# Performance work log

Measured on AMD Instinct MI355X. Metric: run time of the kernel, lower is better.

The kernel has to match this reference:

```python
import jax, jax.numpy as jnp
import numpy as np

B, H, S, D = 2, 16, 2048, 64
N_SINK = 1


def setup_inputs() -> dict:
    key = jax.random.key(0)
    kq, kk, ks = jax.random.split(key, 3)
    q = jax.random.normal(kq, (B, H, S, D), dtype=jnp.float32)
    k = jax.random.normal(kk, (B, H, S, D), dtype=jnp.float32)
    sinks = jax.random.normal(ks, (B, H, S, N_SINK), dtype=jnp.float32)
    return {"q": q, "k": k, "sinks": sinks}


def reference(q, k, sinks):
    # scores: [B,H,S,S] = q @ k^T
    scores = jnp.einsum("bhqd,bhkd->bhqk", q, k)
    # per-key norm ||k||, broadcast over query dim: [B,H,1,S]
    denom = jnp.sqrt(jnp.sum(k * k, axis=-1))[..., None, :]
    w = scores / denom
    # causal: zero (NOT -inf) above the diagonal, faithful to torch.tril
    w = jnp.tril(w)
    # append learned sink logits: [B,H,S,S+N_SINK]
    w = jnp.concatenate([w, sinks], axis=-1)
    return jax.nn.softmax(w, axis=-1)
```

## Files before the change

### kernel.cpp

```cpp
#include <hip/hip_runtime.h>
#include <hip/hip_fp16.h>
#include <math.h>

#define S 2048
#define D 64
#define BH 32
#define TILE 64
#define NT (S / TILE)
#define SP1 (S + 1)

typedef _Float16 f16;
typedef f16 f16x8 __attribute__((ext_vector_type(8)));
typedef f16 f16x4 __attribute__((ext_vector_type(4)));
typedef float f32x4 __attribute__((ext_vector_type(4)));

struct __attribute__((packed, aligned(4))) f4u { float x, y, z, w; };

#define LDS_PITCH 72

__global__ __launch_bounds__(256) void knorm_kernel(const float* __restrict__ k,
                                                    float* __restrict__ rinv) {
    int row  = (blockIdx.x * 256 + threadIdx.x) >> 6;
    int lane = threadIdx.x & 63;
    float v = k[(size_t)row * D + lane];
    float s = v * v;
    #pragma unroll
    for (int off = 32; off; off >>= 1) s += __shfl_xor(s, off);
    if (lane == 0) rinv[row] = 1.0f / sqrtf(s);
}

__global__ __launch_bounds__(256) void fused_kernel(
    const float* __restrict__ q, const float* __restrict__ k,
    const float* __restrict__ sinks, const float* __restrict__ rinv,
    float* __restrict__ out)
{
    __shared__ __align__(16) f16 qs[TILE * LDS_PITCH];
    __shared__ __align__(16) f16 ks[2][TILE * LDS_PITCH];
    __shared__ float ils[TILE];

    const int it = NT - 1 - blockIdx.x;
    const int bh = blockIdx.y;
    const int i0 = it * TILE;
    const int tid  = threadIdx.x;
    const int lane = tid & 63;
    const int w    = tid >> 6;
    const int m    = lane & 15;
    const int quad = lane >> 4;
    const int sr   = tid >> 4;
    const int sc4  = (tid & 15) * 4;

    const float* qbase = q + (size_t)bh * S * D;
    const float* kbase = k + (size_t)bh * S * D;
    const float* rbase = rinv + (size_t)bh * S;
    float* obase = out + (size_t)bh * S * SP1;

    float4 pre[4];

    auto loadk = [&](int jt) {
        const float* tb = kbase + (size_t)(jt * TILE) * D;
        #pragma unroll
        for (int rb = 0; rb < 4; rb++)
            pre[rb] = *(const float4*)(tb + (size_t)(rb * 16 + sr) * D + sc4);
    };
    auto writek = [&](int buf) {
        #pragma unroll
        for (int rb = 0; rb < 4; rb++) {
            float4 v = pre[rb];
            f16x4 hv; hv[0] = (f16)v.x; hv[1] = (f16)v.y; hv[2] = (f16)v.z; hv[3] = (f16)v.w;
            *(f16x4*)&ks[buf][(rb * 16 + sr) * LDS_PITCH + sc4] = hv;
        }
    };

    loadk(0);
    {
        #pragma unroll
        for (int rb = 0; rb < 4; rb++) {
            int row = rb * 16 + sr;
            float4 v = *(const float4*)(qbase + (size_t)(i0 + row) * D + sc4);
            f16x4 hv; hv[0] = (f16)v.x; hv[1] = (f16)v.y; hv[2] = (f16)v.z; hv[3] = (f16)v.w;
            *(f16x4*)&qs[row * LDS_PITCH + sc4] = hv;
        }
    }
    writek(0);
    __syncthreads();

    f16x8 a0 = *(const f16x8*)&qs[(w * 16 + m) * LDS_PITCH + 0  + quad * 8];
    f16x8 a1 = *(const f16x8*)&qs[(w * 16 + m) * LDS_PITCH + 32 + quad * 8];

    const int ib = i0 + w * 16 + quad * 4;

    float rowsum[4] = {0.f, 0.f, 0.f, 0.f};
    for (int jt = 0; jt <= it; jt++) {
        if (jt < it) loadk(jt + 1);
        const int buf = jt & 1;
        const bool diag = (jt == it);
        const int j0 = jt * TILE;
        #pragma unroll
        for (int st = 0; st < 4; st++) {
            f16x8 b0 = *(const f16x8*)&ks[buf][(st * 16 + m) * LDS_PITCH + 0  + quad * 8];
            f16x8 b1 = *(const f16x8*)&ks[buf][(st * 16 + m) * LDS_PITCH + 32 + quad * 8];
            f32x4 acc = {0.f, 0.f, 0.f, 0.f};
            acc = __builtin_amdgcn_mfma_f32_16x16x32_f16(a0, b0, acc, 0, 0, 0);
            acc = __builtin_amdgcn_mfma_f32_16x16x32_f16(a1, b1, acc, 0, 0, 0);
            const int j = j0 + st * 16 + m;
            const float rj = rbase[j];
            #pragma unroll
            for (int r = 0; r < 4; r++) {
                float e = __expf(acc[r] * rj);
                if (diag && j > ib + r) e = 0.0f;
                rowsum[r] += e;
            }
        }
        if (jt < it) writek((jt + 1) & 1);
        __syncthreads();
    }

    #pragma unroll
    for (int off = 1; off < 16; off <<= 1)
        #pragma unroll
        for (int r = 0; r < 4; r++) rowsum[r] += __shfl_xor(rowsum[r], off);

    if (m == 0) {
        #pragma unroll
        for (int r = 0; r < 4; r++) {
            int i = ib + r;
            float l = rowsum[r] + (float)(S - 1 - i) + __expf(sinks[bh * S + i]);
            ils[w * 16 + quad * 4 + r] = 1.0f / l;
        }
    }
    __syncthreads();

    if (tid < TILE) {
        int i = i0 + tid;
        obase[(size_t)i * SP1 + S] = __expf(sinks[bh * S + i]) * ils[tid];
    }

    float il[4];
    #pragma unroll
    for (int r = 0; r < 4; r++) il[r] = ils[w * 16 + quad * 4 + r];

    for (int jt = it; jt >= 0; jt--) {
        if (jt > 0) loadk(jt - 1);
        const int buf = jt & 1;
        const bool diag = (jt == it);
        const int j0 = jt * TILE;
        #pragma unroll
        for (int st = 0; st < 4; st++) {
            f16x8 b0 = *(const f16x8*)&ks[buf][(st * 16 + m) * LDS_PITCH + 0  + quad * 8];
            f16x8 b1 = *(const f16x8*)&ks[buf][(st * 16 + m) * LDS_PITCH + 32 + quad * 8];
            f32x4 acc = {0.f, 0.f, 0.f, 0.f};
            acc = __builtin_amdgcn_mfma_f32_16x16x32_f16(a0, b0, acc, 0, 0, 0);
            acc = __builtin_amdgcn_mfma_f32_16x16x32_f16(a1, b1, acc, 0, 0, 0);
            const int j = j0 + st * 16 + m;
            const float rj = rbase[j];
            #pragma unroll
            for (int r = 0; r < 4; r++) {
                float val = __expf(acc[r] * rj) * il[r];
                if (diag && j > ib + r) val = il[r];
                obase[(size_t)(ib + r) * SP1 + j] = val;
            }
        }
        if (jt > 0) writek((jt - 1) & 1);
        __syncthreads();
    }

    for (int jt = it + 1; jt < NT; jt++) {
        const int j0 = jt * TILE;
        #pragma unroll
        for (int rb = 0; rb < 4; rb++) {
            int row = w * 16 + rb * 4 + (lane >> 4);
            float v = ils[row];
            f4u vv = {v, v, v, v};
            *(f4u*)&obase[(size_t)(i0 + row) * SP1 + j0 + (lane & 15) * 4] = vv;
        }
    }
}

extern "C" void kernel_launch(void* const* d_in, const int* in_sizes, int n_in,
                              void* d_out, int out_size, void* d_ws, size_t ws_size,
                              hipStream_t stream) {
    const float* q     = (const float*)d_in[0];
    const float* k     = (const float*)d_in[1];
    const float* sinks = (const float*)d_in[2];
    float* out = (float*)d_out;

    float* rinv = (float*)d_ws;

    knorm_kernel<<<dim3(BH * S / 4), 256, 0, stream>>>(k, rinv);
    fused_kernel<<<dim3(NT, BH), 256, 0, stream>>>(q, k, sinks, rinv, out);
}
```

Measured before the change: 697.6 us.

## Pre-scale K to fp16 with folded norm, transpose MFMA for vectorized output stores

K is normalized, multiplied by log2(e) and converted to fp16 in a prep kernel, and Q is converted to fp16 in a separate prep kernel. The fused kernel then loads half-precision tiles directly, with no per-element rinv lookup, and uses exp2. The MFMA operands are swapped so each lane owns one query row and four consecutive keys, which allows a single 16-byte store per lane in the output pass instead of four scattered scalar stores. This adds an extra launch and a workspace round trip, and rounds the normalization and scale factor into fp16 K, which can slightly change accuracy.

```diff
diff --git a/kernel.cpp b/kernel.cpp
--- a/kernel.cpp
+++ b/kernel.cpp
@@ -8,6 +8,7 @@
 #define TILE 64
 #define NT (S / TILE)
 #define SP1 (S + 1)
+#define LOG2E 1.44269504088896f
 
 typedef _Float16 f16;
 typedef f16 f16x8 __attribute__((ext_vector_type(8)));
@@ -18,21 +19,31 @@
 
 #define LDS_PITCH 72
 
-__global__ __launch_bounds__(256) void knorm_kernel(const float* __restrict__ k,
-                                                    float* __restrict__ rinv) {
+__global__ __launch_bounds__(256) void prep_k(const float* __restrict__ k,
+                                              f16* __restrict__ kh) {
     int row  = (blockIdx.x * 256 + threadIdx.x) >> 6;
     int lane = threadIdx.x & 63;
     float v = k[(size_t)row * D + lane];
     float s = v * v;
     #pragma unroll
     for (int off = 32; off; off >>= 1) s += __shfl_xor(s, off);
-    if (lane == 0) rinv[row] = 1.0f / sqrtf(s);
+    kh[(size_t)row * D + lane] = (f16)(v * (1.0f / sqrtf(s)) * LOG2E);
+}
+
+__global__ __launch_bounds__(256) void prep_q(const float* __restrict__ q,
+                                              f16* __restrict__ qh) {
+    size_t t = (size_t)blockIdx.x * 256 + threadIdx.x;
+    const float4* src = (const float4*)(q + t * 8);
+    float4 v0 = src[0], v1 = src[1];
+    f16x8 h;
+    h[0] = (f16)v0.x; h[1] = (f16)v0.y; h[2] = (f16)v0.z; h[3] = (f16)v0.w;
+    h[4] = (f16)v1.x; h[5] = (f16)v1.y; h[6] = (f16)v1.z; h[7] = (f16)v1.w;
+    *(f16x8*)(qh + t * 8) = h;
 }
 
 __global__ __launch_bounds__(256) void fused_kernel(
-    const float* __restrict__ q, const float* __restrict__ k,
-    const float* __restrict__ sinks, const float* __restrict__ rinv,
-    float* __restrict__ out)
+    const f16* __restrict__ qh, const f16* __restrict__ kh,
+    const float* __restrict__ sinks, float* __restrict__ out)
 {
     __shared__ __align__(16) f16 qs[TILE * LDS_PITCH];
     __shared__ __align__(16) f16 ks[2][TILE * LDS_PITCH];
@@ -46,50 +57,40 @@
     const int w    = tid >> 6;
     const int m    = lane & 15;
     const int quad = lane >> 4;
-    const int sr   = tid >> 4;
-    const int sc4  = (tid & 15) * 4;
+    const int srow = tid >> 2;
+    const int sc   = (tid & 3) * 16;
 
-    const float* qbase = q + (size_t)bh * S * D;
-    const float* kbase = k + (size_t)bh * S * D;
-    const float* rbase = rinv + (size_t)bh * S;
+    const f16* qb = qh + (size_t)bh * S * D;
+    const f16* kb = kh + (size_t)bh * S * D;
     float* obase = out + (size_t)bh * S * SP1;
 
-    float4 pre[4];
+    f16x8 pre0, pre1;
 
     auto loadk = [&](int jt) {
-        const float* tb = kbase + (size_t)(jt * TILE) * D;
-        #pragma unroll
-        for (int rb = 0; rb < 4; rb++)
-            pre[rb] = *(const float4*)(tb + (size_t)(rb * 16 + sr) * D + sc4);
+        const f16* tb = kb + (size_t)(jt * TILE + srow) * D + sc;
+        pre0 = *(const f16x8*)tb;
+        pre1 = *(const f16x8*)(tb + 8);
     };
     auto writek = [&](int buf) {
-        #pragma unroll
-        for (int rb = 0; rb < 4; rb++) {
-            float4 v = pre[rb];
-            f16x4 hv; hv[0] = (f16)v.x; hv[1] = (f16)v.y; hv[2] = (f16)v.z; hv[3] = (f16)v.w;
-            *(f16x4*)&ks[buf][(rb * 16 + sr) * LDS_PITCH + sc4] = hv;
-        }
+        *(f16x8*)&ks[buf][srow * LDS_PITCH + sc]     = pre0;
+        *(f16x8*)&ks[buf][srow * LDS_PITCH + sc + 8] = pre1;
     };
 
     loadk(0);
     {
-        #pragma unroll
-        for (int rb = 0; rb < 4; rb++) {
-            int row = rb * 16 + sr;
-            float4 v = *(const float4*)(qbase + (size_t)(i0 + row) * D + sc4);
-            f16x4 hv; hv[0] = (f16)v.x; hv[1] = (f16)v.y; hv[2] = (f16)v.z; hv[3] = (f16)v.w;
-            *(f16x4*)&qs[row * LDS_PITCH + sc4] = hv;
-        }
+        const f16* tb = qb + (size_t)(i0 + srow) * D + sc;
+        *(f16x8*)&qs[srow * LDS_PITCH + sc]     = *(const f16x8*)tb;
+        *(f16x8*)&qs[srow * LDS_PITCH + sc + 8] = *(const f16x8*)(tb + 8);
     }
     writek(0);
     __syncthreads();
 
-    f16x8 a0 = *(const f16x8*)&qs[(w * 16 + m) * LDS_PITCH + 0  + quad * 8];
-    f16x8 a1 = *(const f16x8*)&qs[(w * 16 + m) * LDS_PITCH + 32 + quad * 8];
+    f16x8 b0 = *(const f16x8*)&qs[(w * 16 + m) * LDS_PITCH + 0  + quad * 8];
+    f16x8 b1 = *(const f16x8*)&qs[(w * 16 + m) * LDS_PITCH + 32 + quad * 8];
 
-    const int ib = i0 + w * 16 + quad * 4;
+    const int iq = i0 + w * 16 + m;
 
-    float rowsum[4] = {0.f, 0.f, 0.f, 0.f};
+    float rowsum = 0.f;
     for (int jt = 0; jt <= it; jt++) {
         if (jt < it) loadk(jt + 1);
         const int buf = jt & 1;
@@ -97,36 +98,29 @@
         const int j0 = jt * TILE;
         #pragma unroll
         for (int st = 0; st < 4; st++) {
-            f16x8 b0 = *(const f16x8*)&ks[buf][(st * 16 + m) * LDS_PITCH + 0  + quad * 8];
-            f16x8 b1 = *(const f16x8*)&ks[buf][(st * 16 + m) * LDS_PITCH + 32 + quad * 8];
+            f16x8 a0 = *(const f16x8*)&ks[buf][(st * 16 + m) * LDS_PITCH + 0  + quad * 8];
+            f16x8 a1 = *(const f16x8*)&ks[buf][(st * 16 + m) * LDS_PITCH + 32 + quad * 8];
             f32x4 acc = {0.f, 0.f, 0.f, 0.f};
             acc = __builtin_amdgcn_mfma_f32_16x16x32_f16(a0, b0, acc, 0, 0, 0);
             acc = __builtin_amdgcn_mfma_f32_16x16x32_f16(a1, b1, acc, 0, 0, 0);
-            const int j = j0 + st * 16 + m;
-            const float rj = rbase[j];
+            const int jb = j0 + st * 16 + quad * 4;
             #pragma unroll
             for (int r = 0; r < 4; r++) {
-                float e = __expf(acc[r] * rj);
-                if (diag && j > ib + r) e = 0.0f;
-                rowsum[r] += e;
+                float e = exp2f(acc[r]);
+                if (diag && (jb + r) > iq) e = 0.0f;
+                rowsum += e;
             }
         }
         if (jt < it) writek((jt + 1) & 1);
         __syncthreads();
     }
 
-    #pragma unroll
-    for (int off = 1; off < 16; off <<= 1)
-        #pragma unroll
-        for (int r = 0; r < 4; r++) rowsum[r] += __shfl_xor(rowsum[r], off);
+    rowsum += __shfl_xor(rowsum, 16);
+    rowsum += __shfl_xor(rowsum, 32);
 
-    if (m == 0) {
-        #pragma unroll
-        for (int r = 0; r < 4; r++) {
-            int i = ib + r;
-            float l = rowsum[r] + (float)(S - 1 - i) + __expf(sinks[bh * S + i]);
-            ils[w * 16 + quad * 4 + r] = 1.0f / l;
-        }
+    if (lane < 16) {
+        float l = rowsum + (float)(S - 1 - iq) + __expf(sinks[bh * S + iq]);
+        ils[w * 16 + m] = 1.0f / l;
     }
     __syncthreads();
 
@@ -135,9 +129,7 @@
         obase[(size_t)i * SP1 + S] = __expf(sinks[bh * S + i]) * ils[tid];
     }
 
-    float il[4];
-    #pragma unroll
-    for (int r = 0; r < 4; r++) il[r] = ils[w * 16 + quad * 4 + r];
+    const float il = ils[w * 16 + m];
 
     for (int jt = it; jt >= 0; jt--) {
         if (jt > 0) loadk(jt - 1);
@@ -146,19 +138,20 @@
         const int j0 = jt * TILE;
         #pragma unroll
         for (int st = 0; st < 4; st++) {
-            f16x8 b0 = *(const f16x8*)&ks[buf][(st * 16 + m) * LDS_PITCH + 0  + quad * 8];
-            f16x8 b1 = *(const f16x8*)&ks[buf][(st * 16 + m) * LDS_PITCH + 32 + quad * 8];
+            f16x8 a0 = *(const f16x8*)&ks[buf][(st * 16 + m) * LDS_PITCH + 0  + quad * 8];
+            f16x8 a1 = *(const f16x8*)&ks[buf][(st * 16 + m) * LDS_PITCH + 32 + quad * 8];
             f32x4 acc = {0.f, 0.f, 0.f, 0.f};
             acc = __builtin_amdgcn_mfma_f32_16x16x32_f16(a0, b0, acc, 0, 0, 0);
             acc = __builtin_amdgcn_mfma_f32_16x16x32_f16(a1, b1, acc, 0, 0, 0);
-            const int j = j0 + st * 16 + m;
-            const float rj = rbase[j];
+            const int jb = j0 + st * 16 + quad * 4;
+            float v[4];
             #pragma unroll
             for (int r = 0; r < 4; r++) {
-                float val = __expf(acc[r] * rj) * il[r];
-                if (diag && j > ib + r) val = il[r];
-                obase[(size_t)(ib + r) * SP1 + j] = val;
+                v[r] = exp2f(acc[r]) * il;
+                if (diag && (jb + r) > iq) v[r] = il;
             }
+            f4u vv = {v[0], v[1], v[2], v[3]};
+            *(f4u*)&obase[(size_t)iq * SP1 + jb] = vv;
         }
         if (jt > 0) writek((jt - 1) & 1);
         __syncthreads();
@@ -168,10 +161,10 @@
         const int j0 = jt * TILE;
         #pragma unroll
         for (int rb = 0; rb < 4; rb++) {
-            int row = w * 16 + rb * 4 + (lane >> 4);
+            int row = w * 16 + rb * 4 + quad;
             float v = ils[row];
             f4u vv = {v, v, v, v};
-            *(f4u*)&obase[(size_t)(i0 + row) * SP1 + j0 + (lane & 15) * 4] = vv;
+            *(f4u*)&obase[(size_t)(i0 + row) * SP1 + j0 + m * 4] = vv;
         }
     }
 }
@@ -184,8 +177,10 @@
     const float* sinks = (const float*)d_in[2];
     float* out = (float*)d_out;
 
-    float* rinv = (float*)d_ws;
+    f16* kh = (f16*)d_ws;
+    f16* qh = kh + (size_t)BH * S * D;
 
-    knorm_kernel<<<dim3(BH * S / 4), 256, 0, stream>>>(k, rinv);
-    fused_kernel<<<dim3(NT, BH), 256, 0, stream>>>(q, k, sinks, rinv, out);
+    prep_k<<<dim3(BH * S / 4), 256, 0, stream>>>(k, kh);
+    prep_q<<<dim3(BH * S * D / 8 / 256), 256, 0, stream>>>(q, qh);
+    fused_kernel<<<dim3(NT, BH), 256, 0, stream>>>(qh, kh, sinks, out);
 }
```

Result: faster. 683.5 us (-2.0%).
